# Kernel tuning notes

Measured on AMD Instinct MI355X. Metric: run time of the kernel, lower is better.

The kernel has to match this reference:

```python
import jax, jax.numpy as jnp
import numpy as np

B, T, N, D, E = 16, 12, 512, 128, 32  # batch, time, nodes, model_dim, node_emb_dim


def setup_inputs() -> dict:
    key = jax.random.key(0)
    ks = jax.random.split(key, 7)
    return {
        "value": jax.random.normal(ks[0], (B, T, N, D), dtype=jnp.float32),
        "emb": jax.random.normal(ks[1], (T, N, E), dtype=jnp.float32),
        "attn_mask": jax.random.randint(ks[2], (B, N, N), 0, 2, dtype=jnp.int32),
        "W_qk": jax.random.normal(ks[3], (E, D), dtype=jnp.float32) * (1.0 / np.sqrt(E)),
        "b_qk": jax.random.normal(ks[4], (D,), dtype=jnp.float32) * 0.02,
        "W_v": jax.random.normal(ks[5], (D, D), dtype=jnp.float32) * (1.0 / np.sqrt(D)),
        "b_v": jax.random.normal(ks[6], (D,), dtype=jnp.float32) * 0.02,
    }


def reference(value, emb, attn_mask, W_qk, b_qk, W_v, b_v):
    # qk projection shared between query and key: [T, N, D]
    qk = emb @ W_qk + b_qk
    # query: softmax over feature dim D
    q = jax.nn.softmax(qk, axis=-1)                      # [T, N, D]
    # key: transpose then softmax over node dim N
    k = jax.nn.softmax(jnp.swapaxes(qk, -1, -2), axis=-1)  # [T, D, N]
    # value projection (note: out_proj in __init__ is unused in forward)
    v = value @ W_v + b_v                                # [B, T, N, D]
    # batch-independent base attention score, then broadcast over batch
    score = jnp.einsum('tnd,tdm->tnm', q, k)             # [T, N, N]
    score = jnp.broadcast_to(score[None], (value.shape[0],) + score.shape)  # [B, T, N, N]
    # masked fill: mask [B, N, N] -> [B, 1, N, N]
    score = jnp.where(attn_mask[:, None] == 0, jnp.float32(-1e9), score)
    out = jnp.einsum('btnm,btmd->btnd', score, v)         # [B, T, N, D]
    return out
```

## Files before the change

### kernel.cpp

```cpp
#include <hip/hip_runtime.h>

#define B_ 16
#define T_ 12
#define N_ 512
#define D_ 128
#define E_ 32

typedef __attribute__((ext_vector_type(8))) unsigned short u16x8;
typedef __attribute__((ext_vector_type(8))) __bf16 bf16x8;
typedef __attribute__((ext_vector_type(4))) float f32x4;

static __device__ __forceinline__ unsigned short f2bf(float f) {
    unsigned u = __float_as_uint(f);
    unsigned r = (u + 0x7fffu + ((u >> 16) & 1u)) >> 16;
    return (unsigned short)r;
}

__global__ __launch_bounds__(128) void kA1W(const float* __restrict__ emb,
                                            const float* __restrict__ Wqk,
                                            const float* __restrict__ bqk,
                                            float* __restrict__ qk,
                                            unsigned short* __restrict__ qb,
                                            const float* __restrict__ Wv,
                                            unsigned short* __restrict__ WvT) {
    if (blockIdx.x >= 6144) {
        int i = (blockIdx.x - 6144) * 128 + threadIdx.x;
        int d = i >> 7, k = i & 127;
        WvT[d * 128 + k] = f2bf(Wv[k * 128 + d]);
        return;
    }
    int tn = blockIdx.x;
    int d  = threadIdx.x;
    __shared__ float es[E_];
    if (d < E_) es[d] = emb[tn * E_ + d];
    __syncthreads();
    float acc = bqk[d];
#pragma unroll
    for (int e = 0; e < E_; ++e) acc = fmaf(es[e], Wqk[e * D_ + d], acc);
    qk[(size_t)tn * D_ + d] = acc;

    int wv = d >> 6, lane = d & 63;
    float mx = acc;
#pragma unroll
    for (int s = 32; s > 0; s >>= 1) mx = fmaxf(mx, __shfl_xor(mx, s));
    __shared__ float wred[2][2];
    if (lane == 0) wred[0][wv] = mx;
    __syncthreads();
    mx = fmaxf(wred[0][0], wred[0][1]);
    float ex = __expf(acc - mx);
    float sum = ex;
#pragma unroll
    for (int s = 32; s > 0; s >>= 1) sum += __shfl_xor(sum, s);
    if (lane == 0) wred[1][wv] = sum;
    __syncthreads();
    sum = wred[1][0] + wred[1][1];
    qb[(size_t)tn * D_ + d] = f2bf(ex / sum);
}

__global__ __launch_bounds__(256) void kA2n(const float* __restrict__ qk,
                                            unsigned short* __restrict__ kN) {
    int t = blockIdx.x >> 4;
    int d0 = (blockIdx.x & 15) * 8;
    int tid = threadIdx.x;
    int dc = tid & 7, ni = tid >> 3;
    const float* base = qk + (size_t)t * N_ * D_ + d0 + dc;
    float vals[16];
    float mx = -1e30f;
#pragma unroll
    for (int j = 0; j < 16; ++j) {
        vals[j] = base[(size_t)(ni + 32 * j) * D_];
        mx = fmaxf(mx, vals[j]);
    }
#pragma unroll
    for (int s = 8; s < 64; s <<= 1) mx = fmaxf(mx, __shfl_xor(mx, s));
    __shared__ float red[2][4][8];
    int wv = tid >> 6;
    if ((tid & 63) < 8) red[0][wv][dc] = mx;
    __syncthreads();
    mx = fmaxf(fmaxf(red[0][0][dc], red[0][1][dc]),
               fmaxf(red[0][2][dc], red[0][3][dc]));
    float sum = 0.f;
#pragma unroll
    for (int j = 0; j < 16; ++j) {
        vals[j] = __expf(vals[j] - mx);
        sum += vals[j];
    }
#pragma unroll
    for (int s = 8; s < 64; s <<= 1) sum += __shfl_xor(sum, s);
    if ((tid & 63) < 8) red[1][wv][dc] = sum;
    __syncthreads();
    sum = red[1][0][dc] + red[1][1][dc] + red[1][2][dc] + red[1][3][dc];
    float inv = 1.f / sum;
    unsigned short* op = kN + (size_t)t * N_ * D_ + d0 + dc;
#pragma unroll
    for (int j = 0; j < 16; ++j)
        op[(size_t)(ni + 32 * j) * D_] = f2bf(vals[j] * inv);
}

__global__ __launch_bounds__(256) void kF(const unsigned short* __restrict__ qb,
                                          const unsigned short* __restrict__ kN,
                                          unsigned short* __restrict__ sc,
                                          const float* __restrict__ value,
                                          const unsigned short* __restrict__ WvT,
                                          const float* __restrict__ bv,
                                          unsigned short* __restrict__ vT,
                                          const int* __restrict__ mask,
                                          unsigned* __restrict__ mb) {
    __shared__ unsigned short shl[2][128 * 72];
    int bid = blockIdx.x;
    int tid = threadIdx.x;

    if (bid >= 960) {
        int o = (bid - 960) * 256 + tid;
        const int* mp = mask + (size_t)o * 32;
        unsigned bits = 0;
#pragma unroll
        for (int j = 0; j < 32; j += 4) {
            int4 m4 = *(const int4*)&mp[j];
            bits |= (m4.x ? 1u : 0u) << j;
            bits |= (m4.y ? 1u : 0u) << (j + 1);
            bits |= (m4.z ? 1u : 0u) << (j + 2);
            bits |= (m4.w ? 1u : 0u) << (j + 3);
        }
        mb[o] = bits;
        return;
    }

    int wave = tid >> 6, lane = tid & 63;
    int q = lane >> 4, lr = lane & 15;
    int rbase = (wave & 1) * 64, cbase = (wave >> 1) * 64;

    f32x4 acc[4][4];
#pragma unroll
    for (int i = 0; i < 4; ++i)
#pragma unroll
        for (int j = 0; j < 4; ++j) acc[i][j] = (f32x4){0.f, 0.f, 0.f, 0.f};

    if (bid < 192) {
        int mt = bid & 3, nt = (bid >> 2) & 3, t = bid >> 4;
        int n0 = nt * 128, m0 = mt * 128;
        unsigned short* Qs = shl[0];
        unsigned short* Ks = shl[1];
        const unsigned short* qp = qb + (size_t)t * N_ * D_ + (size_t)n0 * D_;
        const unsigned short* kp = kN + (size_t)t * N_ * D_ + (size_t)m0 * D_;

        for (int c = 0; c < 2; ++c) {
            int k0 = c * 64;
            __syncthreads();
#pragma unroll
            for (int i = 0; i < 4; ++i) {
                int lin = tid + i * 256;
                int r = lin >> 3, seg = lin & 7;
                *(u16x8*)&Qs[r * 72 + seg * 8] =
                    *(const u16x8*)&qp[(size_t)r * D_ + k0 + seg * 8];
                *(u16x8*)&Ks[r * 72 + seg * 8] =
                    *(const u16x8*)&kp[(size_t)r * D_ + k0 + seg * 8];
            }
            __syncthreads();
#pragma unroll
            for (int kk = 0; kk < 2; ++kk) {
                bf16x8 a[4], b[4];
#pragma unroll
                for (int i = 0; i < 4; ++i)
                    a[i] = *(const bf16x8*)&Qs[(rbase + 16 * i + lr) * 72 + kk * 32 + q * 8];
#pragma unroll
                for (int j = 0; j < 4; ++j)
                    b[j] = *(const bf16x8*)&Ks[(cbase + 16 * j + lr) * 72 + kk * 32 + q * 8];
#pragma unroll
                for (int i = 0; i < 4; ++i)
#pragma unroll
                    for (int j = 0; j < 4; ++j)
                        acc[i][j] = __builtin_amdgcn_mfma_f32_16x16x32_bf16(
                            a[i], b[j], acc[i][j], 0, 0, 0);
            }
        }
        unsigned short* sp = sc + (size_t)t * N_ * N_;
#pragma unroll
        for (int i = 0; i < 4; ++i)
#pragma unroll
            for (int j = 0; j < 4; ++j) {
                int row0 = n0 + rbase + 16 * i + q * 4;
                int col = m0 + cbase + 16 * j + lr;
#pragma unroll
                for (int e = 0; e < 4; ++e)
                    sp[(size_t)(row0 + e) * N_ + col] = f2bf(acc[i][j][e]);
            }
        return;
    }

    {
        int idx = bid - 192;
        int mt = idx & 3, bt = idx >> 2;
        int m0 = mt * 128;
        unsigned short* Ws = shl[0];
        unsigned short* Vs = shl[1];
        const float* vp = value + ((size_t)bt * N_ + m0) * D_;

        for (int c = 0; c < 2; ++c) {
            int k0 = c * 64;
            __syncthreads();
#pragma unroll
            for (int i = 0; i < 4; ++i) {
                int lin = tid + i * 256;
                int r = lin >> 3, seg = lin & 7;
                *(u16x8*)&Ws[r * 72 + seg * 8] =
                    *(const u16x8*)&WvT[r * 128 + k0 + seg * 8];
            }
#pragma unroll
            for (int i = 0; i < 8; ++i) {
                int lin = tid + i * 256;
                int r = lin >> 4, c4 = lin & 15;
                float4 f = *(const float4*)&vp[(size_t)r * D_ + k0 + c4 * 4];
                ushort4 o;
                o.x = f2bf(f.x); o.y = f2bf(f.y); o.z = f2bf(f.z); o.w = f2bf(f.w);
                *(ushort4*)&Vs[r * 72 + c4 * 4] = o;
            }
            __syncthreads();
#pragma unroll
            for (int kk = 0; kk < 2; ++kk) {
                bf16x8 a[4], b[4];
#pragma unroll
                for (int i = 0; i < 4; ++i)
                    a[i] = *(const bf16x8*)&Ws[(rbase + 16 * i + lr) * 72 + kk * 32 + q * 8];
#pragma unroll
                for (int j = 0; j < 4; ++j)
                    b[j] = *(const bf16x8*)&Vs[(cbase + 16 * j + lr) * 72 + kk * 32 + q * 8];
#pragma unroll
                for (int i = 0; i < 4; ++i)
#pragma unroll
                    for (int j = 0; j < 4; ++j)
                        acc[i][j] = __builtin_amdgcn_mfma_f32_16x16x32_bf16(
                            a[i], b[j], acc[i][j], 0, 0, 0);
            }
        }
        unsigned short* op = vT + (size_t)bt * N_ * D_;
#pragma unroll
        for (int i = 0; i < 4; ++i) {
            int row0 = rbase + 16 * i + q * 4;
#pragma unroll
            for (int j = 0; j < 4; ++j) {
                int col = m0 + cbase + 16 * j + lr;
#pragma unroll
                for (int e = 0; e < 4; ++e)
                    op[(size_t)(row0 + e) * N_ + col] = f2bf(acc[i][j][e] + bv[row0 + e]);
            }
        }
    }
}

__global__ __launch_bounds__(256, 3) void kC(const unsigned short* __restrict__ sc,
                                             const unsigned* __restrict__ mb,
                                             const unsigned short* __restrict__ vT,
                                             float* __restrict__ out) {
    int n0 = blockIdx.x * 128;
    int t = blockIdx.y, b = blockIdx.z;
    int tid = threadIdx.x;
    int wave = tid >> 6, lane = tid & 63;
    int q = lane >> 4, lr = lane & 15;
    int rbase = (wave & 1) * 64, cbase = (wave >> 1) * 64;

    __shared__ unsigned short Sb[128 * 64];
    __shared__ unsigned short Vb[2][128 * 64];

    const unsigned short* scp = sc + (size_t)t * N_ * N_ + (size_t)n0 * N_;
    const unsigned short* vtp = vT + ((size_t)(b * T_ + t)) * N_ * D_;
    const unsigned* mbp = mb + ((size_t)b * N_ + n0) * 16;
    const unsigned short NEG = 0xCE6E;

    f32x4 acc[4][4];
#pragma unroll
    for (int i = 0; i < 4; ++i)
#pragma unroll
        for (int j = 0; j < 4; ++j) acc[i][j] = (f32x4){0.f, 0.f, 0.f, 0.f};

    int sr = tid >> 1, sh2 = tid & 1;
    const unsigned short* sg = scp + (size_t)sr * N_ + sh2 * 32;
    const unsigned* mwp = mbp + sr * 16 + sh2;
    int swz_r = (sr & 7) << 4;
    char* Sw[4];
#pragma unroll
    for (int p = 0; p < 4; ++p)
        Sw[p] = (char*)Sb + sr * 128 + ((sh2 * 64 + p * 16) ^ swz_r);

    int l3 = lane >> 3, l7 = lane & 7;
    int vin = (l7 * 16) ^ (l3 << 4);
    const char* vbase = (const char*)vtp;

#pragma unroll
    for (int it = 0; it < 4; ++it) {
        int row = (it * 4 + wave) * 8 + l3;
        const char* src = vbase + (size_t)row * 1024 + vin;
        char* dst = (char*)&Vb[0][0] + ((it * 4 + wave) * 64 + lane) * 16;
        __builtin_amdgcn_global_load_lds(
            (const __attribute__((address_space(1))) unsigned*)src,
            (__attribute__((address_space(3))) unsigned*)dst, 16, 0, 0);
    }
    u16x8 sreg[4];
    unsigned mw;
#pragma unroll
    for (int p = 0; p < 4; ++p) sreg[p] = *(const u16x8*)(sg + p * 8);
    mw = mwp[0];

    for (int kc = 0; kc < 8; ++kc) {
        int cur = kc & 1;
#pragma unroll
        for (int p = 0; p < 4; ++p) {
            unsigned bits = mw >> (p * 8);
            u16x8 o;
#pragma unroll
            for (int j = 0; j < 8; ++j)
                o[j] = ((bits >> j) & 1u) ? sreg[p][j] : NEG;
            *(u16x8*)Sw[p] = o;
        }
        if (kc < 7) {
            int off = (kc + 1) * 128;
#pragma unroll
            for (int it = 0; it < 4; ++it) {
                int row = (it * 4 + wave) * 8 + l3;
                const char* src = vbase + (size_t)row * 1024 + off + vin;
                char* dst = (char*)&Vb[cur ^ 1][0] + ((it * 4 + wave) * 64 + lane) * 16;
                __builtin_amdgcn_global_load_lds(
                    (const __attribute__((address_space(1))) unsigned*)src,
                    (__attribute__((address_space(3))) unsigned*)dst, 16, 0, 0);
            }
            int eoff = (kc + 1) * 64;
#pragma unroll
            for (int p = 0; p < 4; ++p) sreg[p] = *(const u16x8*)(sg + eoff + p * 8);
            mw = mwp[(kc + 1) * 2];
        }
        asm volatile("s_waitcnt lgkmcnt(0)" ::: "memory");
        __builtin_amdgcn_s_barrier();
        __builtin_amdgcn_sched_barrier(0);
        {
            const char* Sbase = (const char*)Sb;
            const char* Vbase = (const char*)&Vb[cur][0];
            int swz_l = (lr & 7) << 4;
#pragma unroll
            for (int ks = 0; ks < 2; ++ks) {
                bf16x8 a[4], bb[4];
#pragma unroll
                for (int i = 0; i < 4; ++i) {
                    int r = rbase + 16 * i + lr;
                    a[i] = *(const bf16x8*)(Sbase + r * 128 + ((ks * 64 + q * 16) ^ swz_l));
                }
#pragma unroll
                for (int j = 0; j < 4; ++j) {
                    int d = cbase + 16 * j + lr;
                    bb[j] = *(const bf16x8*)(Vbase + d * 128 + ((ks * 64 + q * 16) ^ swz_l));
                }
#pragma unroll
                for (int i = 0; i < 4; ++i)
#pragma unroll
                    for (int j = 0; j < 4; ++j)
                        acc[i][j] = __builtin_amdgcn_mfma_f32_16x16x32_bf16(
                            a[i], bb[j], acc[i][j], 0, 0, 0);
            }
        }
        __builtin_amdgcn_s_barrier();
        __builtin_amdgcn_sched_barrier(0);
    }

    float* ob = out + ((size_t)(b * T_ + t)) * N_ * D_;
#pragma unroll
    for (int i = 0; i < 4; ++i) {
#pragma unroll
        for (int j = 0; j < 4; ++j) {
            int row0 = n0 + rbase + 16 * i + q * 4;
            int col = cbase + 16 * j + lr;
#pragma unroll
            for (int e = 0; e < 4; ++e)
                ob[(size_t)(row0 + e) * D_ + col] = acc[i][j][e];
        }
    }
}

extern "C" void kernel_launch(void* const* d_in, const int* in_sizes, int n_in,
                              void* d_out, int out_size, void* d_ws, size_t ws_size,
                              hipStream_t stream) {
    const float* value = (const float*)d_in[0];
    const float* emb   = (const float*)d_in[1];
    const int*   mask  = (const int*)d_in[2];
    const float* Wqk   = (const float*)d_in[3];
    const float* bqk   = (const float*)d_in[4];
    const float* Wv    = (const float*)d_in[5];
    const float* bvv   = (const float*)d_in[6];
    float* out = (float*)d_out;

    float* ws = (float*)d_ws;
    float*          qkf  = ws;
    unsigned short* qb   = (unsigned short*)(ws + 786432);
    unsigned short* kNb  = (unsigned short*)(ws + 1179648);
    unsigned short* scb  = (unsigned short*)(ws + 1572864);
    unsigned short* vtb  = (unsigned short*)(ws + 3145728);
    unsigned short* WvTb = (unsigned short*)(ws + 9437184);
    unsigned*       mbp  = (unsigned*)(ws + 9445376);

    kA1W<<<6272, 128, 0, stream>>>(emb, Wqk, bqk, qkf, qb, Wv, WvTb);
    kA2n<<<192, 256, 0, stream>>>(qkf, kNb);
    kF<<<1472, 256, 0, stream>>>(qb, kNb, scb, value, WvTb, bvv, vtb, mask, mbp);
    kC<<<dim3(4, T_, B_), 256, 0, stream>>>(scb, mbp, vtb, out);
}
```

Baseline: 161.8 us.

## Restructure prologue kernels: batched qk rows, single-stage swizzled LDS loads, relocate mask packing

kA1 now computes 8 (t,n) rows per block, holding Wqk columns in registers and reducing the softmax entirely within a wave instead of through shared memory and barriers. The mask bit-packing moves from kF into kA1. kF now loads the full K=128 tiles in one stage using global_load_lds with an XOR swizzle instead of two staged chunks with padded LDS. It also gets a launch-bounds occupancy hint and vectorised bias loads. The aim is to cut launch, barrier and memory-latency overhead in the small prologue kernels, at the cost of more register pressure and larger LDS tiles per block.

```diff
diff --git a/kernel.cpp b/kernel.cpp
--- a/kernel.cpp
+++ b/kernel.cpp
@@ -16,45 +16,75 @@
     return (unsigned short)r;
 }
 
-__global__ __launch_bounds__(128) void kA1W(const float* __restrict__ emb,
-                                            const float* __restrict__ Wqk,
-                                            const float* __restrict__ bqk,
-                                            float* __restrict__ qk,
-                                            unsigned short* __restrict__ qb,
-                                            const float* __restrict__ Wv,
-                                            unsigned short* __restrict__ WvT) {
-    if (blockIdx.x >= 6144) {
-        int i = (blockIdx.x - 6144) * 128 + threadIdx.x;
+static __device__ __forceinline__ void gld16(const void* src, void* dst) {
+    __builtin_amdgcn_global_load_lds(
+        (const __attribute__((address_space(1))) unsigned*)src,
+        (__attribute__((address_space(3))) unsigned*)dst, 16, 0, 0);
+}
+
+__global__ __launch_bounds__(128) void kA1(const float* __restrict__ emb,
+                                           const float* __restrict__ Wqk,
+                                           const float* __restrict__ bqk,
+                                           float* __restrict__ qk,
+                                           unsigned short* __restrict__ qb,
+                                           const float* __restrict__ Wv,
+                                           unsigned short* __restrict__ WvT,
+                                           const int* __restrict__ mask,
+                                           unsigned* __restrict__ mb) {
+    int bid = blockIdx.x;
+    int tid = threadIdx.x;
+    if (bid >= 896) {
+        int o = (bid - 896) * 128 + tid;
+        const int* mp = mask + (size_t)o * 32;
+        unsigned bits = 0;
+#pragma unroll
+        for (int j = 0; j < 32; j += 4) {
+            int4 m4 = *(const int4*)&mp[j];
+            bits |= (m4.x ? 1u : 0u) << j;
+            bits |= (m4.y ? 1u : 0u) << (j + 1);
+            bits |= (m4.z ? 1u : 0u) << (j + 2);
+            bits |= (m4.w ? 1u : 0u) << (j + 3);
+        }
+        mb[o] = bits;
+        return;
+    }
+    if (bid >= 768) {
+        int i = (bid - 768) * 128 + tid;
         int d = i >> 7, k = i & 127;
         WvT[d * 128 + k] = f2bf(Wv[k * 128 + d]);
         return;
     }
-    int tn = blockIdx.x;
-    int d  = threadIdx.x;
-    __shared__ float es[E_];
-    if (d < E_) es[d] = emb[tn * E_ + d];
-    __syncthreads();
-    float acc = bqk[d];
-#pragma unroll
-    for (int e = 0; e < E_; ++e) acc = fmaf(es[e], Wqk[e * D_ + d], acc);
-    qk[(size_t)tn * D_ + d] = acc;
-
-    int wv = d >> 6, lane = d & 63;
-    float mx = acc;
-#pragma unroll
-    for (int s = 32; s > 0; s >>= 1) mx = fmaxf(mx, __shfl_xor(mx, s));
-    __shared__ float wred[2][2];
-    if (lane == 0) wred[0][wv] = mx;
-    __syncthreads();
-    mx = fmaxf(wred[0][0], wred[0][1]);
-    float ex = __expf(acc - mx);
-    float sum = ex;
-#pragma unroll
-    for (int s = 32; s > 0; s >>= 1) sum += __shfl_xor(sum, s);
-    if (lane == 0) wred[1][wv] = sum;
-    __syncthreads();
-    sum = wred[1][0] + wred[1][1];
-    qb[(size_t)tn * D_ + d] = f2bf(ex / sum);
+    int w = tid >> 6, l = tid & 63;
+    float wq0[E_], wq1[E_];
+#pragma unroll
+    for (int e = 0; e < E_; ++e) {
+        wq0[e] = Wqk[e * D_ + l];
+        wq1[e] = Wqk[e * D_ + l + 64];
+    }
+    float b0 = bqk[l], b1 = bqk[l + 64];
+    for (int rr = 0; rr < 4; ++rr) {
+        int tn = bid * 8 + w * 4 + rr;
+        const float* ep = emb + (size_t)tn * E_;
+        float a0 = b0, a1 = b1;
+#pragma unroll
+        for (int e = 0; e < E_; ++e) {
+            float ev = ep[e];
+            a0 = fmaf(ev, wq0[e], a0);
+            a1 = fmaf(ev, wq1[e], a1);
+        }
+        qk[(size_t)tn * D_ + l] = a0;
+        qk[(size_t)tn * D_ + l + 64] = a1;
+        float mx = fmaxf(a0, a1);
+#pragma unroll
+        for (int s = 32; s > 0; s >>= 1) mx = fmaxf(mx, __shfl_xor(mx, s));
+        float e0 = __expf(a0 - mx), e1 = __expf(a1 - mx);
+        float sum = e0 + e1;
+#pragma unroll
+        for (int s = 32; s > 0; s >>= 1) sum += __shfl_xor(sum, s);
+        float inv = 1.f / sum;
+        qb[(size_t)tn * D_ + l] = f2bf(e0 * inv);
+        qb[(size_t)tn * D_ + l + 64] = f2bf(e1 * inv);
+    }
 }
 
 __global__ __launch_bounds__(256) void kA2n(const float* __restrict__ qk,
@@ -97,38 +127,21 @@
         op[(size_t)(ni + 32 * j) * D_] = f2bf(vals[j] * inv);
 }
 
-__global__ __launch_bounds__(256) void kF(const unsigned short* __restrict__ qb,
-                                          const unsigned short* __restrict__ kN,
-                                          unsigned short* __restrict__ sc,
-                                          const float* __restrict__ value,
-                                          const unsigned short* __restrict__ WvT,
-                                          const float* __restrict__ bv,
-                                          unsigned short* __restrict__ vT,
-                                          const int* __restrict__ mask,
-                                          unsigned* __restrict__ mb) {
-    __shared__ unsigned short shl[2][128 * 72];
+__global__ __launch_bounds__(256, 2) void kF(const unsigned short* __restrict__ qb,
+                                             const unsigned short* __restrict__ kN,
+                                             unsigned short* __restrict__ sc,
+                                             const float* __restrict__ value,
+                                             const unsigned short* __restrict__ WvT,
+                                             const float* __restrict__ bv,
+                                             unsigned short* __restrict__ vT) {
+    __shared__ unsigned short shA[128 * 128];
+    __shared__ unsigned short shB[128 * 128];
     int bid = blockIdx.x;
     int tid = threadIdx.x;
-
-    if (bid >= 960) {
-        int o = (bid - 960) * 256 + tid;
-        const int* mp = mask + (size_t)o * 32;
-        unsigned bits = 0;
-#pragma unroll
-        for (int j = 0; j < 32; j += 4) {
-            int4 m4 = *(const int4*)&mp[j];
-            bits |= (m4.x ? 1u : 0u) << j;
-            bits |= (m4.y ? 1u : 0u) << (j + 1);
-            bits |= (m4.z ? 1u : 0u) << (j + 2);
-            bits |= (m4.w ? 1u : 0u) << (j + 3);
-        }
-        mb[o] = bits;
-        return;
-    }
-
     int wave = tid >> 6, lane = tid & 63;
     int q = lane >> 4, lr = lane & 15;
     int rbase = (wave & 1) * 64, cbase = (wave >> 1) * 64;
+    int il = lane >> 4, i16 = lane & 15;
 
     f32x4 acc[4][4];
 #pragma unroll
@@ -139,40 +152,40 @@
     if (bid < 192) {
         int mt = bid & 3, nt = (bid >> 2) & 3, t = bid >> 4;
         int n0 = nt * 128, m0 = mt * 128;
-        unsigned short* Qs = shl[0];
-        unsigned short* Ks = shl[1];
-        const unsigned short* qp = qb + (size_t)t * N_ * D_ + (size_t)n0 * D_;
-        const unsigned short* kp = kN + (size_t)t * N_ * D_ + (size_t)m0 * D_;
-
-        for (int c = 0; c < 2; ++c) {
-            int k0 = c * 64;
-            __syncthreads();
+        const char* qp = (const char*)(qb + (size_t)t * N_ * D_ + (size_t)n0 * D_);
+        const char* kp = (const char*)(kN + (size_t)t * N_ * D_ + (size_t)m0 * D_);
+#pragma unroll
+        for (int it = 0; it < 8; ++it) {
+            int r = it * 16 + wave * 4 + il;
+            int si = (i16 * 16) ^ ((r & 15) << 4);
+            char* dA = (char*)shA + (it * 16 + wave * 4) * 256 + lane * 16;
+            char* dB = (char*)shB + (it * 16 + wave * 4) * 256 + lane * 16;
+            gld16(qp + (size_t)r * 256 + si, dA);
+            gld16(kp + (size_t)r * 256 + si, dB);
+        }
+        asm volatile("s_waitcnt vmcnt(0)" ::: "memory");
+        __builtin_amdgcn_s_barrier();
+        const char* Ab = (const char*)shA;
+        const char* Bb = (const char*)shB;
+#pragma unroll
+        for (int ks = 0; ks < 4; ++ks) {
+            bf16x8 a[4], b[4];
 #pragma unroll
             for (int i = 0; i < 4; ++i) {
-                int lin = tid + i * 256;
-                int r = lin >> 3, seg = lin & 7;
-                *(u16x8*)&Qs[r * 72 + seg * 8] =
-                    *(const u16x8*)&qp[(size_t)r * D_ + k0 + seg * 8];
-                *(u16x8*)&Ks[r * 72 + seg * 8] =
-                    *(const u16x8*)&kp[(size_t)r * D_ + k0 + seg * 8];
-            }
-            __syncthreads();
-#pragma unroll
-            for (int kk = 0; kk < 2; ++kk) {
-                bf16x8 a[4], b[4];
-#pragma unroll
-                for (int i = 0; i < 4; ++i)
-                    a[i] = *(const bf16x8*)&Qs[(rbase + 16 * i + lr) * 72 + kk * 32 + q * 8];
+                int r = rbase + 16 * i + lr;
+                a[i] = *(const bf16x8*)(Ab + r * 256 + ((ks * 64 + q * 16) ^ ((r & 15) << 4)));
+            }
+#pragma unroll
+            for (int j = 0; j < 4; ++j) {
+                int r = cbase + 16 * j + lr;
+                b[j] = *(const bf16x8*)(Bb + r * 256 + ((ks * 64 + q * 16) ^ ((r & 15) << 4)));
+            }
+#pragma unroll
+            for (int i = 0; i < 4; ++i)
 #pragma unroll
                 for (int j = 0; j < 4; ++j)
-                    b[j] = *(const bf16x8*)&Ks[(cbase + 16 * j + lr) * 72 + kk * 32 + q * 8];
-#pragma unroll
-                for (int i = 0; i < 4; ++i)
-#pragma unroll
-                    for (int j = 0; j < 4; ++j)
-                        acc[i][j] = __builtin_amdgcn_mfma_f32_16x16x32_bf16(
-                            a[i], b[j], acc[i][j], 0, 0, 0);
-            }
+                    acc[i][j] = __builtin_amdgcn_mfma_f32_16x16x32_bf16(
+                        a[i], b[j], acc[i][j], 0, 0, 0);
         }
         unsigned short* sp = sc + (size_t)t * N_ * N_;
 #pragma unroll
@@ -192,57 +205,69 @@
         int idx = bid - 192;
         int mt = idx & 3, bt = idx >> 2;
         int m0 = mt * 128;
-        unsigned short* Ws = shl[0];
-        unsigned short* Vs = shl[1];
         const float* vp = value + ((size_t)bt * N_ + m0) * D_;
-
-        for (int c = 0; c < 2; ++c) {
-            int k0 = c * 64;
-            __syncthreads();
+        const char* wp = (const char*)WvT;
+
+        int g = tid >> 4, c16 = tid & 15;
+        float4 vv[16];
+#pragma unroll
+        for (int j = 0; j < 16; ++j) {
+            int r = g * 8 + (j >> 1);
+            int kf = (j & 1) * 64 + c16 * 4;
+            vv[j] = *(const float4*)(vp + (size_t)r * D_ + kf);
+        }
+#pragma unroll
+        for (int it = 0; it < 8; ++it) {
+            int r = it * 16 + wave * 4 + il;
+            int si = (i16 * 16) ^ ((r & 15) << 4);
+            char* dA = (char*)shA + (it * 16 + wave * 4) * 256 + lane * 16;
+            gld16(wp + (size_t)r * 256 + si, dA);
+        }
+#pragma unroll
+        for (int j = 0; j < 16; ++j) {
+            int r = g * 8 + (j >> 1);
+            int kb = (j & 1) * 128 + c16 * 8;
+            ushort4 o;
+            o.x = f2bf(vv[j].x); o.y = f2bf(vv[j].y);
+            o.z = f2bf(vv[j].z); o.w = f2bf(vv[j].w);
+            *(ushort4*)((char*)shB + r * 256 + (kb ^ ((r & 15) << 4))) = o;
+        }
+        asm volatile("s_waitcnt vmcnt(0) lgkmcnt(0)" ::: "memory");
+        __builtin_amdgcn_s_barrier();
+        const char* Ab = (const char*)shA;
+        const char* Bb = (const char*)shB;
+#pragma unroll
+        for (int ks = 0; ks < 4; ++ks) {
+            bf16x8 a[4], b[4];
 #pragma unroll
             for (int i = 0; i < 4; ++i) {
-                int lin = tid + i * 256;
-                int r = lin >> 3, seg = lin & 7;
-                *(u16x8*)&Ws[r * 72 + seg * 8] =
-                    *(const u16x8*)&WvT[r * 128 + k0 + seg * 8];
-            }
-#pragma unroll
-            for (int i = 0; i < 8; ++i) {
-                int lin = tid + i * 256;
-                int r = lin >> 4, c4 = lin & 15;
-                float4 f = *(const float4*)&vp[(size_t)r * D_ + k0 + c4 * 4];
-                ushort4 o;
-                o.x = f2bf(f.x); o.y = f2bf(f.y); o.z = f2bf(f.z); o.w = f2bf(f.w);
-                *(ushort4*)&Vs[r * 72 + c4 * 4] = o;
-            }
-            __syncthreads();
-#pragma unroll
-            for (int kk = 0; kk < 2; ++kk) {
-                bf16x8 a[4], b[4];
-#pragma unroll
-                for (int i = 0; i < 4; ++i)
-                    a[i] = *(const bf16x8*)&Ws[(rbase + 16 * i + lr) * 72 + kk * 32 + q * 8];
+                int r = rbase + 16 * i + lr;
+                a[i] = *(const bf16x8*)(Ab + r * 256 + ((ks * 64 + q * 16) ^ ((r & 15) << 4)));
+            }
+#pragma unroll
+            for (int j = 0; j < 4; ++j) {
+                int r = cbase + 16 * j + lr;
+                b[j] = *(const bf16x8*)(Bb + r * 256 + ((ks * 64 + q * 16) ^ ((r & 15) << 4)));
+            }
+#pragma unroll
+            for (int i = 0; i < 4; ++i)
 #pragma unroll
                 for (int j = 0; j < 4; ++j)
-                    b[j] = *(const bf16x8*)&Vs[(cbase + 16 * j + lr) * 72 + kk * 32 + q * 8];
-#pragma unroll
-                for (int i = 0; i < 4; ++i)
-#pragma unroll
-                    for (int j = 0; j < 4; ++j)
-                        acc[i][j] = __builtin_amdgcn_mfma_f32_16x16x32_bf16(
-                            a[i], b[j], acc[i][j], 0, 0, 0);
-            }
+                    acc[i][j] = __builtin_amdgcn_mfma_f32_16x16x32_bf16(
+                        a[i], b[j], acc[i][j], 0, 0, 0);
         }
         unsigned short* op = vT + (size_t)bt * N_ * D_;
 #pragma unroll
         for (int i = 0; i < 4; ++i) {
             int row0 = rbase + 16 * i + q * 4;
+            float4 bq = *(const float4*)&bv[row0];
 #pragma unroll
             for (int j = 0; j < 4; ++j) {
                 int col = m0 + cbase + 16 * j + lr;
-#pragma unroll
-                for (int e = 0; e < 4; ++e)
-                    op[(size_t)(row0 + e) * N_ + col] = f2bf(acc[i][j][e] + bv[row0 + e]);
+                op[(size_t)(row0 + 0) * N_ + col] = f2bf(acc[i][j][0] + bq.x);
+                op[(size_t)(row0 + 1) * N_ + col] = f2bf(acc[i][j][1] + bq.y);
+                op[(size_t)(row0 + 2) * N_ + col] = f2bf(acc[i][j][2] + bq.z);
+                op[(size_t)(row0 + 3) * N_ + col] = f2bf(acc[i][j][3] + bq.w);
             }
         }
     }
@@ -291,9 +316,7 @@
         int row = (it * 4 + wave) * 8 + l3;
         const char* src = vbase + (size_t)row * 1024 + vin;
         char* dst = (char*)&Vb[0][0] + ((it * 4 + wave) * 64 + lane) * 16;
-        __builtin_amdgcn_global_load_lds(
-            (const __attribute__((address_space(1))) unsigned*)src,
-            (__attribute__((address_space(3))) unsigned*)dst, 16, 0, 0);
+        gld16(src, dst);
     }
     u16x8 sreg[4];
     unsigned mw;
@@ -319,9 +342,7 @@
                 int row = (it * 4 + wave) * 8 + l3;
                 const char* src = vbase + (size_t)row * 1024 + off + vin;
                 char* dst = (char*)&Vb[cur ^ 1][0] + ((it * 4 + wave) * 64 + lane) * 16;
-                __builtin_amdgcn_global_load_lds(
-                    (const __attribute__((address_space(1))) unsigned*)src,
-                    (__attribute__((address_space(3))) unsigned*)dst, 16, 0, 0);
+                gld16(src, dst);
             }
             int eoff = (kc + 1) * 64;
 #pragma unroll
@@ -395,8 +416,8 @@
     unsigned short* WvTb = (unsigned short*)(ws + 9437184);
     unsigned*       mbp  = (unsigned*)(ws + 9445376);
 
-    kA1W<<<6272, 128, 0, stream>>>(emb, Wqk, bqk, qkf, qb, Wv, WvTb);
+    kA1<<<1920, 128, 0, stream>>>(emb, Wqk, bqk, qkf, qb, Wv, WvTb, mask, mbp);
     kA2n<<<192, 256, 0, stream>>>(qkf, kNb);
-    kF<<<1472, 256, 0, stream>>>(qb, kNb, scb, value, WvTb, bvv, vtb, mask, mbp);
+    kF<<<960, 256, 0, stream>>>(qb, kNb, scb, value, WvTb, bvv, vtb);
     kC<<<dim3(4, T_, B_), 256, 0, stream>>>(scb, mbp, vtb, out);
 }
```

New measurement: 160.5 us. About the same (-0.8%).
